# Kernel optimization log

Hardware: AMD Instinct MI355X
Metric: run time of the kernel (lower is better)

## Reference

```python
import jax, jax.numpy as jnp
import numpy as np

N = 10000          # nodes
E = 160000         # edges (before self-loops)
F_IN = 256
H, C = 8, 64       # heads, channels per head
NUM_CLASSES = 40
NEG_SLOPE = 0.2    # PyG GATConv default leaky_relu slope


def setup_inputs() -> dict:
    key = jax.random.key(0)
    ks = jax.random.split(key, 16)
    s = 0.1  # keep logits tame
    x = jax.random.normal(ks[0], (N, F_IN), jnp.float32)
    edge_index = jax.random.randint(ks[1], (2, E), 0, N)
    W0 = jax.random.normal(ks[2], (F_IN, H * C), jnp.float32) / np.sqrt(F_IN)
    a_src0 = jax.random.normal(ks[3], (H, C), jnp.float32) * s
    a_dst0 = jax.random.normal(ks[4], (H, C), jnp.float32) * s
    b0 = jnp.zeros((H * C,), jnp.float32)
    W1 = jax.random.normal(ks[5], (H * C, H * C), jnp.float32) / np.sqrt(H * C)
    a_src1 = jax.random.normal(ks[6], (H, C), jnp.float32) * s
    a_dst1 = jax.random.normal(ks[7], (H, C), jnp.float32) * s
    b1 = jnp.zeros((H * C,), jnp.float32)
    W2 = jax.random.normal(ks[8], (H * C, NUM_CLASSES), jnp.float32) / np.sqrt(H * C)
    a_src2 = jax.random.normal(ks[9], (1, NUM_CLASSES), jnp.float32) * s
    a_dst2 = jax.random.normal(ks[10], (1, NUM_CLASSES), jnp.float32) * s
    b2 = jnp.zeros((NUM_CLASSES,), jnp.float32)
    return dict(x=x, edge_index=edge_index, W0=W0, a_src0=a_src0, a_dst0=a_dst0, b0=b0,
                W1=W1, a_src1=a_src1, a_dst1=a_dst1, b1=b1,
                W2=W2, a_src2=a_src2, a_dst2=a_dst2, b2=b2)


def gat_conv(x, src, dst, W, a_src, a_dst, b, concat):
    """PyG GATConv (eval mode: dropout = identity)."""
    n = x.shape[0]
    h, c = a_src.shape
    hx = (x @ W).reshape(n, h, c)                       # [N,H,C]
    al_s = jnp.sum(hx * a_src, axis=-1)                 # [N,H]
    al_d = jnp.sum(hx * a_dst, axis=-1)                 # [N,H]
    e = jax.nn.leaky_relu(al_s[src] + al_d[dst], NEG_SLOPE)  # [E,H]
    # neighbor softmax over incoming edges of each dst node
    m = jax.ops.segment_max(e, dst, num_segments=n)     # [N,H]
    ex = jnp.exp(e - m[dst])
    denom = jax.ops.segment_sum(ex, dst, num_segments=n)
    alpha = ex / (denom[dst] + 1e-16)                   # [E,H]
    msg = hx[src] * alpha[:, :, None]                   # [E,H,C]
    out = jax.ops.segment_sum(msg, dst, num_segments=n) # [N,H,C]
    out = out.reshape(n, h * c) if concat else out.mean(axis=1)
    return out + b


def reference(x, edge_index, W0, a_src0, a_dst0, b0, W1, a_src1, a_dst1, b1,
              W2, a_src2, a_dst2, b2):
    # add self-loops once (PyG GATConv add_self_loops=True)
    loops = jnp.arange(N, dtype=edge_index.dtype)
    src = jnp.concatenate([edge_index[0], loops])
    dst = jnp.concatenate([edge_index[1], loops])
    x = jax.nn.elu(gat_conv(x, src, dst, W0, a_src0, a_dst0, b0, True))
    x = jax.nn.elu(gat_conv(x, src, dst, W1, a_src1, a_dst1, b1, True))
    return gat_conv(x, src, dst, W2, a_src2, a_dst2, b2, False)
```

## Files before the change

### kernel.cpp

```cpp
#include <hip/hip_runtime.h>
#include <math.h>

#define NN 10000
#define EE 160000
#define ET 170000
#define FIN 256
#define HH 8
#define CC 64
#define HC 512
#define NCLS 40
#define ELLW 96

typedef unsigned short u16;
typedef unsigned int u32;
typedef _Float16 f16;
using f16x8 = __attribute__((ext_vector_type(8))) _Float16;
using f32x4 = __attribute__((ext_vector_type(4))) float;

#define MFMA16(a, b, c) __builtin_amdgcn_mfma_f32_16x16x32_f16((a), (b), (c), 0, 0, 0)

__global__ __launch_bounds__(256) void convW_kernel(const float* __restrict__ W0,
                                                    const float* __restrict__ W1,
                                                    const float* __restrict__ W2,
                                                    f16* __restrict__ w0T,
                                                    f16* __restrict__ w1T,
                                                    f16* __restrict__ w2T,
                                                    int* __restrict__ cnt) {
    int i = blockIdx.x * 256 + threadIdx.x;
    if (i < NN) cnt[i] = 0;
    if (i < HC * FIN) {
        int n = i >> 8, k = i & 255;
        w0T[i] = (f16)W0[(size_t)k * HC + n];
    } else if (i < HC * FIN + HC * HC) {
        int j = i - HC * FIN;
        int n = j >> 9, k = j & 511;
        w1T[j] = (f16)W1[(size_t)k * HC + n];
    } else if (i < HC * FIN + HC * HC + NCLS * HC) {
        int j = i - HC * FIN - HC * HC;
        int n = j >> 9, k = j & 511;
        w2T[j] = (f16)W2[(size_t)k * NCLS + n];
    }
}

__global__ __launch_bounds__(256) void scatter_ell(const int* __restrict__ ei,
                                                   int* __restrict__ cnt,
                                                   int* __restrict__ ell) {
    int e = blockIdx.x * 256 + threadIdx.x;
    if (e >= ET) return;
    int s, d;
    if (e < EE) { s = ei[e]; d = ei[EE + e]; }
    else        { s = e - EE; d = s; }
    int pos = atomicAdd(&cnt[d], 1);
    if (pos < ELLW) ell[(size_t)d * ELLW + pos] = s;
}

template <int K, bool AF32>
__global__ __launch_bounds__(512) void gemm_attn(const void* __restrict__ Aptr,
                                                 const f16* __restrict__ BT,
                                                 const float* __restrict__ a_src,
                                                 const float* __restrict__ a_dst,
                                                 f16* __restrict__ hx2,
                                                 float* __restrict__ al_s,
                                                 float* __restrict__ al_d) {
    constexpr int KK = K / 32;
    constexpr int CH = K / 8;
    __shared__ f16 Bs[64 * K];
    int t = threadIdx.x;
    int hp = blockIdx.x;
    int lane = t & 63, w = t >> 6;
    int fm = lane & 15, g = lane >> 4;
    int bm = blockIdx.y * 128 + w * 16;
    int row = bm + fm;
    bool rok = row < NN;

    f16x8 af[KK];
    if (AF32) {
        const float* A = (const float*)Aptr;
#pragma unroll
        for (int kk = 0; kk < KK; ++kk) {
            float4 lo = make_float4(0.f, 0.f, 0.f, 0.f), hi = lo;
            if (rok) {
                const float* ap = A + (size_t)row * K + kk * 32 + g * 8;
                lo = *(const float4*)ap;
                hi = *(const float4*)(ap + 4);
            }
            f16x8 v;
            v[0] = (f16)lo.x; v[1] = (f16)lo.y; v[2] = (f16)lo.z; v[3] = (f16)lo.w;
            v[4] = (f16)hi.x; v[5] = (f16)hi.y; v[6] = (f16)hi.z; v[7] = (f16)hi.w;
            af[kk] = v;
        }
    } else {
        const f16* A = (const f16*)Aptr;
#pragma unroll
        for (int kk = 0; kk < KK; ++kk) {
            uint4 r = rok ? *(const uint4*)(A + (size_t)row * K + kk * 32 + g * 8)
                          : make_uint4(0u, 0u, 0u, 0u);
            af[kk] = __builtin_bit_cast(f16x8, r);
        }
    }

    for (int sl = 0; sl < 2; ++sl) {
        int h = hp * 2 + sl;
        const f16* bsrc = BT + (size_t)h * 64 * K;
        for (int c = t; c < 64 * CH; c += 512) {
            int brow = c / CH;
            int j = c - brow * CH;
            uint4 v = *(const uint4*)(bsrc + (size_t)brow * K + j * 8);
            *(uint4*)&Bs[(size_t)brow * K + ((j ^ (brow & 7)) * 8)] = v;
        }
        __syncthreads();

        f32x4 acc[4] = {};
#pragma unroll
        for (int kk = 0; kk < KK; ++kk) {
#pragma unroll
            for (int nt = 0; nt < 4; ++nt) {
                f16x8 b = *(const f16x8*)
                    &Bs[(nt * 16 + fm) * K + (((kk * 4 + g) ^ (fm & 7)) * 8)];
                acc[nt] = MFMA16(af[kk], b, acc[nt]);
            }
        }

        float asc[4], adc[4];
#pragma unroll
        for (int nt = 0; nt < 4; ++nt) {
            asc[nt] = a_src[h * 64 + nt * 16 + fm];
            adc[nt] = a_dst[h * 64 + nt * 16 + fm];
        }
#pragma unroll
        for (int r = 0; r < 4; ++r) {
            int orow = bm + g * 4 + r;
            float s = acc[0][r] * asc[0] + acc[1][r] * asc[1] +
                      acc[2][r] * asc[2] + acc[3][r] * asc[3];
            float d = acc[0][r] * adc[0] + acc[1][r] * adc[1] +
                      acc[2][r] * adc[2] + acc[3][r] * adc[3];
#pragma unroll
            for (int off = 1; off < 16; off <<= 1) {
                s += __shfl_xor(s, off);
                d += __shfl_xor(d, off);
            }
            if (orow < NN) {
                if (fm == 0) {
                    al_s[orow * 8 + h] = s;
                    al_d[orow * 8 + h] = d;
                }
#pragma unroll
                for (int nt = 0; nt < 4; ++nt)
                    hx2[(size_t)orow * HC + h * 64 + nt * 16 + fm] =
                        (f16)acc[nt][r];
            }
        }
        __syncthreads();
    }
}

__global__ __launch_bounds__(256) void gemm2_attn(const f16* __restrict__ A,
                                                  const f16* __restrict__ BT,
                                                  const float* __restrict__ a_src2,
                                                  const float* __restrict__ a_dst2,
                                                  float* __restrict__ hx40,
                                                  float* __restrict__ als2,
                                                  float* __restrict__ ald2) {
    __shared__ f16 Bs[48 * HC];
    int t = threadIdx.x;
    int lane = t & 63, w = t >> 6;
    int fm = lane & 15, g = lane >> 4;
    int bm = blockIdx.x * 64 + w * 16;
    int row = bm + fm;
    bool rok = row < NN;

    for (int c = t; c < 48 * 64; c += 256) {
        int brow = c >> 6, j = c & 63;
        uint4 v = make_uint4(0u, 0u, 0u, 0u);
        if (brow < NCLS) v = *(const uint4*)(BT + (size_t)brow * HC + j * 8);
        *(uint4*)&Bs[brow * HC + ((j ^ (brow & 7)) * 8)] = v;
    }

    f16x8 af[16];
#pragma unroll
    for (int kk = 0; kk < 16; ++kk) {
        uint4 r = rok ? *(const uint4*)(A + (size_t)row * HC + kk * 32 + g * 8)
                      : make_uint4(0u, 0u, 0u, 0u);
        af[kk] = __builtin_bit_cast(f16x8, r);
    }
    __syncthreads();

    f32x4 acc[3] = {};
#pragma unroll
    for (int kk = 0; kk < 16; ++kk) {
#pragma unroll
        for (int nt = 0; nt < 3; ++nt) {
            f16x8 b = *(const f16x8*)
                &Bs[(nt * 16 + fm) * HC + (((kk * 4 + g) ^ (fm & 7)) * 8)];
            acc[nt] = MFMA16(af[kk], b, acc[nt]);
        }
    }

    float a2s[3], a2d[3];
#pragma unroll
    for (int nt = 0; nt < 3; ++nt) {
        int col = nt * 16 + fm;
        a2s[nt] = (col < NCLS) ? a_src2[col] : 0.f;
        a2d[nt] = (col < NCLS) ? a_dst2[col] : 0.f;
    }
#pragma unroll
    for (int r = 0; r < 4; ++r) {
        int orow = bm + g * 4 + r;
        float s = acc[0][r] * a2s[0] + acc[1][r] * a2s[1] + acc[2][r] * a2s[2];
        float d = acc[0][r] * a2d[0] + acc[1][r] * a2d[1] + acc[2][r] * a2d[2];
#pragma unroll
        for (int off = 1; off < 16; off <<= 1) {
            s += __shfl_xor(s, off);
            d += __shfl_xor(d, off);
        }
        if (orow < NN) {
            if (fm == 0) { als2[orow] = s; ald2[orow] = d; }
#pragma unroll
            for (int nt = 0; nt < 3; ++nt) {
                int col = nt * 16 + fm;
                if (col < NCLS) hx40[(size_t)orow * NCLS + col] = acc[nt][r];
            }
        }
    }
}

__global__ __launch_bounds__(256) void agg_ell(const f16* __restrict__ hx2,
                                               const float* __restrict__ al_s,
                                               const float* __restrict__ al_d,
                                               const int* __restrict__ cnt,
                                               const int* __restrict__ ell,
                                               const float* __restrict__ bias,
                                               f16* __restrict__ outF) {
    __shared__ float accbuf[2][64][8];
    __shared__ float denbuf[2][64];
    int t = threadIdx.x;
    int lane = t & 63, w = t >> 6;
    int p = w >> 1, sub = w & 1;
    int n = blockIdx.x * 2 + p;
    bool nok = n < NN;
    int ch = lane * 8;
    int h = lane >> 3;
    float acc[8] = {0.f, 0.f, 0.f, 0.f, 0.f, 0.f, 0.f, 0.f};
    float den = 0.f;
    if (nok) {
        float ald = al_d[n * HH + h];
        int dg = cnt[n]; if (dg > ELLW) dg = ELLW;
        const int* ep = ell + (size_t)n * ELLW;
        int i = sub;
        for (; i + 6 < dg; i += 8) {
            int s0 = ep[i], s1 = ep[i + 2], s2 = ep[i + 4], s3 = ep[i + 6];
            float e0 = al_s[s0 * HH + h], e1 = al_s[s1 * HH + h];
            float e2 = al_s[s2 * HH + h], e3 = al_s[s3 * HH + h];
            uint4 v0 = *(const uint4*)(hx2 + (size_t)s0 * HC + ch);
            uint4 v1 = *(const uint4*)(hx2 + (size_t)s1 * HC + ch);
            uint4 v2 = *(const uint4*)(hx2 + (size_t)s2 * HC + ch);
            uint4 v3 = *(const uint4*)(hx2 + (size_t)s3 * HC + ch);
            e0 += ald; e0 = e0 > 0.f ? e0 : 0.2f * e0;
            e1 += ald; e1 = e1 > 0.f ? e1 : 0.2f * e1;
            e2 += ald; e2 = e2 > 0.f ? e2 : 0.2f * e2;
            e3 += ald; e3 = e3 > 0.f ? e3 : 0.2f * e3;
            float w0 = __expf(e0), w1 = __expf(e1);
            float w2 = __expf(e2), w3 = __expf(e3);
            f16x8 f0 = __builtin_bit_cast(f16x8, v0);
            f16x8 f1 = __builtin_bit_cast(f16x8, v1);
            f16x8 f2 = __builtin_bit_cast(f16x8, v2);
            f16x8 f3 = __builtin_bit_cast(f16x8, v3);
#pragma unroll
            for (int j = 0; j < 8; ++j)
                acc[j] += w0 * (float)f0[j] + w1 * (float)f1[j] +
                          w2 * (float)f2[j] + w3 * (float)f3[j];
            den += w0 + w1 + w2 + w3;
        }
        for (; i < dg; i += 2) {
            int s = ep[i];
            float e = al_s[s * HH + h] + ald;
            e = e > 0.f ? e : 0.2f * e;
            float wgt = __expf(e);
            uint4 v = *(const uint4*)(hx2 + (size_t)s * HC + ch);
            f16x8 f = __builtin_bit_cast(f16x8, v);
#pragma unroll
            for (int j = 0; j < 8; ++j) acc[j] += wgt * (float)f[j];
            den += wgt;
        }
    }
    if (sub == 1) {
#pragma unroll
        for (int j = 0; j < 8; ++j) accbuf[p][lane][j] = acc[j];
        denbuf[p][lane] = den;
    }
    __syncthreads();
    if (sub == 0 && nok) {
#pragma unroll
        for (int j = 0; j < 8; ++j) acc[j] += accbuf[p][lane][j];
        den += denbuf[p][lane];
        float inv = 1.f / (den + 1e-16f);
        float4 b0v = *(const float4*)(bias + ch);
        float4 b1v = *(const float4*)(bias + ch + 4);
        float bb[8] = {b0v.x, b0v.y, b0v.z, b0v.w, b1v.x, b1v.y, b1v.z, b1v.w};
        f16x8 o;
#pragma unroll
        for (int j = 0; j < 8; ++j) {
            float v = acc[j] * inv + bb[j];
            v = v > 0.f ? v : expm1f(v);
            o[j] = (f16)v;
        }
        *(uint4*)(outF + (size_t)n * HC + ch) = __builtin_bit_cast(uint4, o);
    }
}

__global__ __launch_bounds__(64) void agg2_final(const float* __restrict__ hx40,
                                                 const float* __restrict__ als,
                                                 const float* __restrict__ aldp,
                                                 const int* __restrict__ cnt,
                                                 const int* __restrict__ ell,
                                                 const float* __restrict__ b2,
                                                 float* __restrict__ out) {
    int n = blockIdx.x;
    int c = threadIdx.x;
    float ald = aldp[n];
    int dg = cnt[n]; if (dg > ELLW) dg = ELLW;
    const int* ep = ell + (size_t)n * ELLW;
    float acc = 0.f, den = 0.f;
    int i = 0;
    for (; i + 4 <= dg; i += 4) {
        int s0 = ep[i], s1 = ep[i + 1], s2 = ep[i + 2], s3 = ep[i + 3];
        float e0 = als[s0], e1 = als[s1], e2 = als[s2], e3 = als[s3];
        float v0 = 0.f, v1 = 0.f, v2 = 0.f, v3 = 0.f;
        if (c < NCLS) {
            v0 = hx40[(size_t)s0 * NCLS + c];
            v1 = hx40[(size_t)s1 * NCLS + c];
            v2 = hx40[(size_t)s2 * NCLS + c];
            v3 = hx40[(size_t)s3 * NCLS + c];
        }
        e0 += ald; e0 = e0 > 0.f ? e0 : 0.2f * e0;
        e1 += ald; e1 = e1 > 0.f ? e1 : 0.2f * e1;
        e2 += ald; e2 = e2 > 0.f ? e2 : 0.2f * e2;
        e3 += ald; e3 = e3 > 0.f ? e3 : 0.2f * e3;
        float w0 = __expf(e0), w1 = __expf(e1), w2 = __expf(e2), w3 = __expf(e3);
        acc += w0 * v0 + w1 * v1 + w2 * v2 + w3 * v3;
        den += w0 + w1 + w2 + w3;
    }
    for (; i < dg; ++i) {
        int s = ep[i];
        float e = als[s] + ald;
        e = e > 0.f ? e : 0.2f * e;
        float wgt = __expf(e);
        if (c < NCLS) acc += wgt * hx40[(size_t)s * NCLS + c];
        den += wgt;
    }
    if (c < NCLS) out[(size_t)n * NCLS + c] = acc / (den + 1e-16f) + b2[c];
}

extern "C" void kernel_launch(void* const* d_in, const int* in_sizes, int n_in,
                              void* d_out, int out_size, void* d_ws, size_t ws_size,
                              hipStream_t stream) {
    const float* x   = (const float*)d_in[0];
    const int*   ei  = (const int*)  d_in[1];
    const float* W0  = (const float*)d_in[2];
    const float* as0 = (const float*)d_in[3];
    const float* ad0 = (const float*)d_in[4];
    const float* b0  = (const float*)d_in[5];
    const float* W1  = (const float*)d_in[6];
    const float* as1 = (const float*)d_in[7];
    const float* ad1 = (const float*)d_in[8];
    const float* b1  = (const float*)d_in[9];
    const float* W2  = (const float*)d_in[10];
    const float* as2 = (const float*)d_in[11];
    const float* ad2 = (const float*)d_in[12];
    const float* b2  = (const float*)d_in[13];
    float* out = (float*)d_out;

    char* p = (char*)d_ws;
    int* cnt  = (int*)p; p += 40064;
    int* ell  = (int*)p; p += (size_t)NN * ELLW * 4;
    f16* w0T  = (f16*)p; p += HC * FIN * 2;
    f16* w1T  = (f16*)p; p += HC * HC * 2;
    f16* w2T  = (f16*)p; p += NCLS * HC * 2;
    f16* hxA  = (f16*)p; p += (size_t)NN * HC * 2;
    f16* hxB  = (f16*)p; p += (size_t)NN * HC * 2;
    f16* fA   = (f16*)p; p += (size_t)NN * HC * 2;
    f16* fB   = (f16*)p; p += (size_t)NN * HC * 2;
    float* hx40 = (float*)p; p += (size_t)NN * NCLS * 4;
    float* als0 = (float*)p; p += NN * HH * 4;
    float* ald0 = (float*)p; p += NN * HH * 4;
    float* als1 = (float*)p; p += NN * HH * 4;
    float* ald1 = (float*)p; p += NN * HH * 4;
    float* als2 = (float*)p; p += NN * 4;
    float* ald2 = (float*)p; p += NN * 4;

    const int NBR = (NN + 127) / 128;
    const int NAG = (NN + 1) / 2;
    const int NB2 = (NN + 63) / 64;

    convW_kernel<<<(HC * FIN + HC * HC + NCLS * HC + 255) / 256, 256, 0, stream>>>(
        W0, W1, W2, w0T, w1T, w2T, cnt);
    scatter_ell<<<(ET + 255) / 256, 256, 0, stream>>>(ei, cnt, ell);

    dim3 gA(4, NBR);
    gemm_attn<FIN, true><<<gA, 512, 0, stream>>>(x, w0T, as0, ad0, hxA, als0, ald0);
    agg_ell<<<NAG, 256, 0, stream>>>(hxA, als0, ald0, cnt, ell, b0, fA);
    gemm_attn<HC, false><<<gA, 512, 0, stream>>>(fA, w1T, as1, ad1, hxB, als1, ald1);
    agg_ell<<<NAG, 256, 0, stream>>>(hxB, als1, ald1, cnt, ell, b1, fB);
    gemm2_attn<<<NB2, 256, 0, stream>>>(fB, w2T, as2, ad2, hx40, als2, ald2);
    agg2_final<<<NN, 64, 0, stream>>>(hx40, als2, ald2, cnt, ell, b2, out);
}
```

Baseline: 206.1 us.

## Pre-convert x to fp16 in prep kernel and vectorize ELL index loads

The input features are converted to fp16 once in the prep kernel, alongside the weight transposes. The first GEMM then reads half-width A rows instead of reading fp32 and converting per block, which matters because the grid has 4 column blocks that each re-read A. The aggregation kernels now load neighbor indices four at a time as int4 and split quads between the two sub-warps, with the remainder handled by one of them. This adds an extra fp32 read and fp16 write of x in the prep pass, and the int4 index loads rely on 16-byte alignment of the ELL rows, which holds because the row width is 96.

```diff
diff --git a/kernel.cpp b/kernel.cpp
--- a/kernel.cpp
+++ b/kernel.cpp
@@ -15,30 +15,41 @@
 typedef unsigned int u32;
 typedef _Float16 f16;
 using f16x8 = __attribute__((ext_vector_type(8))) _Float16;
+using f16x4 = __attribute__((ext_vector_type(4))) _Float16;
 using f32x4 = __attribute__((ext_vector_type(4))) float;
 
 #define MFMA16(a, b, c) __builtin_amdgcn_mfma_f32_16x16x32_f16((a), (b), (c), 0, 0, 0)
 
-__global__ __launch_bounds__(256) void convW_kernel(const float* __restrict__ W0,
-                                                    const float* __restrict__ W1,
-                                                    const float* __restrict__ W2,
-                                                    f16* __restrict__ w0T,
-                                                    f16* __restrict__ w1T,
-                                                    f16* __restrict__ w2T,
-                                                    int* __restrict__ cnt) {
+__global__ __launch_bounds__(256) void prep_kernel(const float* __restrict__ x,
+                                                   const float* __restrict__ W0,
+                                                   const float* __restrict__ W1,
+                                                   const float* __restrict__ W2,
+                                                   f16* __restrict__ xh,
+                                                   f16* __restrict__ w0T,
+                                                   f16* __restrict__ w1T,
+                                                   f16* __restrict__ w2T,
+                                                   int* __restrict__ cnt) {
     int i = blockIdx.x * 256 + threadIdx.x;
     if (i < NN) cnt[i] = 0;
-    if (i < HC * FIN) {
-        int n = i >> 8, k = i & 255;
-        w0T[i] = (f16)W0[(size_t)k * HC + n];
-    } else if (i < HC * FIN + HC * HC) {
-        int j = i - HC * FIN;
-        int n = j >> 9, k = j & 511;
-        w1T[j] = (f16)W1[(size_t)k * HC + n];
-    } else if (i < HC * FIN + HC * HC + NCLS * HC) {
-        int j = i - HC * FIN - HC * HC;
-        int n = j >> 9, k = j & 511;
-        w2T[j] = (f16)W2[(size_t)k * NCLS + n];
+    if (i < NN * FIN / 4) {
+        float4 v = ((const float4*)x)[i];
+        f16x4 o;
+        o[0] = (f16)v.x; o[1] = (f16)v.y; o[2] = (f16)v.z; o[3] = (f16)v.w;
+        ((f16x4*)xh)[i] = o;
+    } else {
+        int j = i - NN * FIN / 4;
+        if (j < HC * FIN) {
+            int n = j >> 8, k = j & 255;
+            w0T[j] = (f16)W0[(size_t)k * HC + n];
+        } else if (j < HC * FIN + HC * HC) {
+            int q = j - HC * FIN;
+            int n = q >> 9, k = q & 511;
+            w1T[q] = (f16)W1[(size_t)k * HC + n];
+        } else if (j < HC * FIN + HC * HC + NCLS * HC) {
+            int q = j - HC * FIN - HC * HC;
+            int n = q >> 9, k = q & 511;
+            w2T[q] = (f16)W2[(size_t)k * NCLS + n];
+        }
     }
 }
 
@@ -54,8 +65,8 @@
     if (pos < ELLW) ell[(size_t)d * ELLW + pos] = s;
 }
 
-template <int K, bool AF32>
-__global__ __launch_bounds__(512) void gemm_attn(const void* __restrict__ Aptr,
+template <int K>
+__global__ __launch_bounds__(512) void gemm_attn(const f16* __restrict__ A,
                                                  const f16* __restrict__ BT,
                                                  const float* __restrict__ a_src,
                                                  const float* __restrict__ a_dst,
@@ -74,29 +85,11 @@
     bool rok = row < NN;
 
     f16x8 af[KK];
-    if (AF32) {
-        const float* A = (const float*)Aptr;
-#pragma unroll
-        for (int kk = 0; kk < KK; ++kk) {
-            float4 lo = make_float4(0.f, 0.f, 0.f, 0.f), hi = lo;
-            if (rok) {
-                const float* ap = A + (size_t)row * K + kk * 32 + g * 8;
-                lo = *(const float4*)ap;
-                hi = *(const float4*)(ap + 4);
-            }
-            f16x8 v;
-            v[0] = (f16)lo.x; v[1] = (f16)lo.y; v[2] = (f16)lo.z; v[3] = (f16)lo.w;
-            v[4] = (f16)hi.x; v[5] = (f16)hi.y; v[6] = (f16)hi.z; v[7] = (f16)hi.w;
-            af[kk] = v;
-        }
-    } else {
-        const f16* A = (const f16*)Aptr;
-#pragma unroll
-        for (int kk = 0; kk < KK; ++kk) {
-            uint4 r = rok ? *(const uint4*)(A + (size_t)row * K + kk * 32 + g * 8)
-                          : make_uint4(0u, 0u, 0u, 0u);
-            af[kk] = __builtin_bit_cast(f16x8, r);
-        }
+#pragma unroll
+    for (int kk = 0; kk < KK; ++kk) {
+        uint4 r = rok ? *(const uint4*)(A + (size_t)row * K + kk * 32 + g * 8)
+                      : make_uint4(0u, 0u, 0u, 0u);
+        af[kk] = __builtin_bit_cast(f16x8, r);
     }
 
     for (int sl = 0; sl < 2; ++sl) {
@@ -246,15 +239,15 @@
         float ald = al_d[n * HH + h];
         int dg = cnt[n]; if (dg > ELLW) dg = ELLW;
         const int* ep = ell + (size_t)n * ELLW;
-        int i = sub;
-        for (; i + 6 < dg; i += 8) {
-            int s0 = ep[i], s1 = ep[i + 2], s2 = ep[i + 4], s3 = ep[i + 6];
-            float e0 = al_s[s0 * HH + h], e1 = al_s[s1 * HH + h];
-            float e2 = al_s[s2 * HH + h], e3 = al_s[s3 * HH + h];
-            uint4 v0 = *(const uint4*)(hx2 + (size_t)s0 * HC + ch);
-            uint4 v1 = *(const uint4*)(hx2 + (size_t)s1 * HC + ch);
-            uint4 v2 = *(const uint4*)(hx2 + (size_t)s2 * HC + ch);
-            uint4 v3 = *(const uint4*)(hx2 + (size_t)s3 * HC + ch);
+        int nq = dg >> 2;
+        for (int q = sub; q < nq; q += 2) {
+            int4 ss = *(const int4*)(ep + (q << 2));
+            float e0 = al_s[ss.x * HH + h], e1 = al_s[ss.y * HH + h];
+            float e2 = al_s[ss.z * HH + h], e3 = al_s[ss.w * HH + h];
+            uint4 v0 = *(const uint4*)(hx2 + (size_t)ss.x * HC + ch);
+            uint4 v1 = *(const uint4*)(hx2 + (size_t)ss.y * HC + ch);
+            uint4 v2 = *(const uint4*)(hx2 + (size_t)ss.z * HC + ch);
+            uint4 v3 = *(const uint4*)(hx2 + (size_t)ss.w * HC + ch);
             e0 += ald; e0 = e0 > 0.f ? e0 : 0.2f * e0;
             e1 += ald; e1 = e1 > 0.f ? e1 : 0.2f * e1;
             e2 += ald; e2 = e2 > 0.f ? e2 : 0.2f * e2;
@@ -271,16 +264,18 @@
                           w2 * (float)f2[j] + w3 * (float)f3[j];
             den += w0 + w1 + w2 + w3;
         }
-        for (; i < dg; i += 2) {
-            int s = ep[i];
-            float e = al_s[s * HH + h] + ald;
-            e = e > 0.f ? e : 0.2f * e;
-            float wgt = __expf(e);
-            uint4 v = *(const uint4*)(hx2 + (size_t)s * HC + ch);
-            f16x8 f = __builtin_bit_cast(f16x8, v);
-#pragma unroll
-            for (int j = 0; j < 8; ++j) acc[j] += wgt * (float)f[j];
-            den += wgt;
+        if (sub == (nq & 1)) {
+            for (int i = nq << 2; i < dg; ++i) {
+                int s = ep[i];
+                float e = al_s[s * HH + h] + ald;
+                e = e > 0.f ? e : 0.2f * e;
+                float wgt = __expf(e);
+                uint4 v = *(const uint4*)(hx2 + (size_t)s * HC + ch);
+                f16x8 f = __builtin_bit_cast(f16x8, v);
+#pragma unroll
+                for (int j = 0; j < 8; ++j) acc[j] += wgt * (float)f[j];
+                den += wgt;
+            }
         }
     }
     if (sub == 1) {
@@ -323,14 +318,14 @@
     float acc = 0.f, den = 0.f;
     int i = 0;
     for (; i + 4 <= dg; i += 4) {
-        int s0 = ep[i], s1 = ep[i + 1], s2 = ep[i + 2], s3 = ep[i + 3];
-        float e0 = als[s0], e1 = als[s1], e2 = als[s2], e3 = als[s3];
+        int4 ss = *(const int4*)(ep + i);
+        float e0 = als[ss.x], e1 = als[ss.y], e2 = als[ss.z], e3 = als[ss.w];
         float v0 = 0.f, v1 = 0.f, v2 = 0.f, v3 = 0.f;
         if (c < NCLS) {
-            v0 = hx40[(size_t)s0 * NCLS + c];
-            v1 = hx40[(size_t)s1 * NCLS + c];
-            v2 = hx40[(size_t)s2 * NCLS + c];
-            v3 = hx40[(size_t)s3 * NCLS + c];
+            v0 = hx40[(size_t)ss.x * NCLS + c];
+            v1 = hx40[(size_t)ss.y * NCLS + c];
+            v2 = hx40[(size_t)ss.z * NCLS + c];
+            v3 = hx40[(size_t)ss.w * NCLS + c];
         }
         e0 += ald; e0 = e0 > 0.f ? e0 : 0.2f * e0;
         e1 += ald; e1 = e1 > 0.f ? e1 : 0.2f * e1;
@@ -376,6 +371,7 @@
     f16* w0T  = (f16*)p; p += HC * FIN * 2;
     f16* w1T  = (f16*)p; p += HC * HC * 2;
     f16* w2T  = (f16*)p; p += NCLS * HC * 2;
+    f16* xh   = (f16*)p; p += (size_t)NN * FIN * 2;
     f16* hxA  = (f16*)p; p += (size_t)NN * HC * 2;
     f16* hxB  = (f16*)p; p += (size_t)NN * HC * 2;
     f16* fA   = (f16*)p; p += (size_t)NN * HC * 2;
@@ -391,15 +387,16 @@
     const int NBR = (NN + 127) / 128;
     const int NAG = (NN + 1) / 2;
     const int NB2 = (NN + 63) / 64;
-
-    convW_kernel<<<(HC * FIN + HC * HC + NCLS * HC + 255) / 256, 256, 0, stream>>>(
-        W0, W1, W2, w0T, w1T, w2T, cnt);
+    const int PREP = NN * FIN / 4 + HC * FIN + HC * HC + NCLS * HC;
+
+    prep_kernel<<<(PREP + 255) / 256, 256, 0, stream>>>(
+        x, W0, W1, W2, xh, w0T, w1T, w2T, cnt);
     scatter_ell<<<(ET + 255) / 256, 256, 0, stream>>>(ei, cnt, ell);
 
     dim3 gA(4, NBR);
-    gemm_attn<FIN, true><<<gA, 512, 0, stream>>>(x, w0T, as0, ad0, hxA, als0, ald0);
+    gemm_attn<FIN><<<gA, 512, 0, stream>>>(xh, w0T, as0, ad0, hxA, als0, ald0);
     agg_ell<<<NAG, 256, 0, stream>>>(hxA, als0, ald0, cnt, ell, b0, fA);
-    gemm_attn<HC, false><<<gA, 512, 0, stream>>>(fA, w1T, as1, ad1, hxB, als1, ald1);
+    gemm_attn<HC><<<gA, 512, 0, stream>>>(fA, w1T, as1, ad1, hxB, als1, ald1);
     agg_ell<<<NAG, 256, 0, stream>>>(hxB, als1, ald1, cnt, ell, b1, fB);
     gemm2_attn<<<NB2, 256, 0, stream>>>(fB, w2T, as2, ad2, hx40, als2, ald2);
     agg2_final<<<NN, 64, 0, stream>>>(hx40, als2, ald2, cnt, ell, b2, out);
```

New measurement: 206.5 us. Within noise of the previous version (+0.2%).
